# Performance work log

Measured on AMD Instinct MI355X. Metric: run time of the kernel, lower is better.

## Reference

```python
import jax, jax.numpy as jnp
import numpy as np

VL = 32

def setup_inputs() -> dict:
    key = jax.random.key(0)
    k1, k2, k3 = jax.random.split(key, 3)
    user = jax.random.normal(k1, (16384, 20, VL + 1), dtype=jnp.float32)
    ctx = jax.random.normal(k2, (16384, 10, VL + 1), dtype=jnp.float32)
    doc = jax.random.normal(k3, (16384, 30, VL + 1), dtype=jnp.float32)
    return {"user": user, "ctx": ctx, "doc": doc}

def reference(user, ctx, doc):
    # feats: [B, F, vl+1] where F = total field count across user/ctx/doc
    feats = jnp.concatenate([user, ctx, doc], axis=1)
    v = feats[..., :VL]          # [B, F, vl] latent factors
    linear = feats[..., -1]      # [B, F]   linear term (last column)
    # FM cross term: 0.5 * ((sum_f v)^2 - sum_f v^2), summed over latent dims
    sum_v = jnp.sum(v, axis=1)           # [B, vl]
    sum_v2 = jnp.sum(v * v, axis=1)      # [B, vl]
    cross = 0.5 * jnp.sum(sum_v * sum_v - sum_v2, axis=-1)  # [B]
    logits = cross + jnp.sum(linear, axis=1)                 # [B]
    return jax.nn.sigmoid(logits)
```

## Files before the change

### kernel.cpp

```cpp
#include <hip/hip_runtime.h>
#include <hip/hip_bf16.h>
#include <math.h>


#define NS 16384
#define PPB 4

__global__ __launch_bounds__(128) void fm_kernel(
    const float* __restrict__ user,
    const float* __restrict__ ctx,
    const float* __restrict__ doc,
    float* __restrict__ out) {
  __shared__ float smem[3960];

  const int tid = threadIdx.x;
  const int pair0 = blockIdx.x * PPB;

  float4* su = (float4*)smem;
  float4* sc = (float4*)(smem + 1320);
  float4* sd = (float4*)(smem + 1980);

  const bool pu = (256 + tid) < 330;
  const bool pc = (128 + tid) < 165;
  const bool pd = (384 + tid) < 495;

  float4 r0, r1, r2, r3, r4, r5, r6, r7, r8;

  auto LOAD = [&](int pair) {
    const float4* gu = (const float4*)(user + (size_t)(2 * pair) * 660);
    const float4* gc = (const float4*)(ctx  + (size_t)(2 * pair) * 330);
    const float4* gd = (const float4*)(doc  + (size_t)(2 * pair) * 990);
    r0 = gu[tid];
    r1 = gu[128 + tid];
    if (pu) r2 = gu[256 + tid];
    r3 = gc[tid];
    if (pc) r4 = gc[128 + tid];
    r5 = gd[tid];
    r6 = gd[128 + tid];
    r7 = gd[256 + tid];
    if (pd) r8 = gd[384 + tid];
  };
  auto STORE = [&]() {
    su[tid] = r0;
    su[128 + tid] = r1;
    if (pu) su[256 + tid] = r2;
    sc[tid] = r3;
    if (pc) sc[128 + tid] = r4;
    sd[tid] = r5;
    sd[128 + tid] = r6;
    sd[256 + tid] = r7;
    if (pd) sd[384 + tid] = r8;
  };

  LOAD(pair0);
  STORE();
  __syncthreads();

  const int w = tid >> 6;
  const int l = tid & 63;
  const int h = l >> 5;
  const int e = l & 31;

  const float* mu = smem + w * 660;
  const float* mc = smem + 1320 + w * 330;
  const float* md = smem + 1980 + w * 990;
  const float* p1 = (h ? md : mu) + e;
  const float* p2 = (h ? (md + 660) : mc) + e;

  for (int it = 0; it < PPB; ++it) {
    const bool more = (it + 1 < PPB);
    if (more) LOAD(pair0 + it + 1);

    float sv = 0.f, sv2 = 0.f;
#pragma unroll
    for (int f = 0; f < 20; ++f) {
      float x = p1[f * 33];
      sv += x; sv2 = fmaf(x, x, sv2);
    }
#pragma unroll
    for (int f = 0; f < 10; ++f) {
      float x = p2[f * 33];
      sv += x; sv2 = fmaf(x, x, sv2);
    }

    float lin = 0.f;
    if (h == 0) {
      if (e < 20)      lin = mu[e * 33 + 32];
      else if (e < 30) lin = mc[(e - 20) * 33 + 32];
    } else {
      if (e < 30) lin = md[e * 33 + 32];
    }

    float svT  = sv  + __shfl_xor(sv,  32, 64);
    float sv2T = sv2 + __shfl_xor(sv2, 32, 64);
    float linT = lin + __shfl_xor(lin, 32, 64);
    float part = fmaf(svT, svT, -sv2T);
#pragma unroll
    for (int m = 16; m > 0; m >>= 1) {
      part += __shfl_xor(part, m, 64);
      linT += __shfl_xor(linT, m, 64);
    }
    if (l == 0) {
      float logit = fmaf(0.5f, part, linT);
      out[2 * (pair0 + it) + w] = 1.f / (1.f + expf(-logit));
    }

    if (more) {
      __syncthreads();
      STORE();
      __syncthreads();
    }
  }
}

extern "C" void kernel_launch(void* const* d_in, const int* in_sizes, int n_in,
                              void* d_out, int out_size, void* d_ws, size_t ws_size,
                              hipStream_t stream) {
  const float* user = (const float*)d_in[0];
  const float* ctx  = (const float*)d_in[1];
  const float* doc  = (const float*)d_in[2];
  float* out = (float*)d_out;

  dim3 block(128);
  dim3 grid(NS / 2 / PPB);
  fm_kernel<<<grid, block, 0, stream>>>(user, ctx, doc, out);
}
```

Before: 144.9 us.

## Double-buffer LDS with direct global-to-LDS async loads and larger PPB

Replaces the register-staged global loads and LDS stores with global_load_lds builtins that write straight into a double-buffered shared-memory region. Each wave loads one half (user+ctx or doc) and the next pair is prefetched while the current one is computed, synchronised by vmcnt waits and raw barriers. Pairs per block go from 4 to 8, halving the grid. The goal is to remove the VGPR round trip and one barrier per iteration. The risks are the doubled LDS footprint, fewer blocks, and the ordering of the manual waitcnt.

```diff
diff --git a/kernel.cpp b/kernel.cpp
--- a/kernel.cpp
+++ b/kernel.cpp
@@ -1,75 +1,71 @@
 #include <hip/hip_runtime.h>
-#include <hip/hip_bf16.h>
 #include <math.h>
 
 
 #define NS 16384
-#define PPB 4
+#define PPB 8
+
+__device__ __forceinline__ void glds16(const void* g, void* l) {
+  __builtin_amdgcn_global_load_lds(
+      (const __attribute__((address_space(1))) void*)g,
+      (__attribute__((address_space(3))) void*)l,
+      16, 0, 0);
+}
 
 __global__ __launch_bounds__(128) void fm_kernel(
     const float* __restrict__ user,
     const float* __restrict__ ctx,
     const float* __restrict__ doc,
     float* __restrict__ out) {
-  __shared__ float smem[3960];
+  __shared__ float smem[2 * 3960];
 
-  const int tid = threadIdx.x;
+  const int tid  = threadIdx.x;
+  const int w    = tid >> 6;
+  const int lane = tid & 63;
   const int pair0 = blockIdx.x * PPB;
 
-  float4* su = (float4*)smem;
-  float4* sc = (float4*)(smem + 1320);
-  float4* sd = (float4*)(smem + 1980);
-
-  const bool pu = (256 + tid) < 330;
-  const bool pc = (128 + tid) < 165;
-  const bool pd = (384 + tid) < 495;
-
-  float4 r0, r1, r2, r3, r4, r5, r6, r7, r8;
-
-  auto LOAD = [&](int pair) {
-    const float4* gu = (const float4*)(user + (size_t)(2 * pair) * 660);
-    const float4* gc = (const float4*)(ctx  + (size_t)(2 * pair) * 330);
-    const float4* gd = (const float4*)(doc  + (size_t)(2 * pair) * 990);
-    r0 = gu[tid];
-    r1 = gu[128 + tid];
-    if (pu) r2 = gu[256 + tid];
-    r3 = gc[tid];
-    if (pc) r4 = gc[128 + tid];
-    r5 = gd[tid];
-    r6 = gd[128 + tid];
-    r7 = gd[256 + tid];
-    if (pd) r8 = gd[384 + tid];
-  };
-  auto STORE = [&]() {
-    su[tid] = r0;
-    su[128 + tid] = r1;
-    if (pu) su[256 + tid] = r2;
-    sc[tid] = r3;
-    if (pc) sc[128 + tid] = r4;
-    sd[tid] = r5;
-    sd[128 + tid] = r6;
-    sd[256 + tid] = r7;
-    if (pd) sd[384 + tid] = r8;
+  auto STAGE = [&](int cb, int pair) {
+    float* buf = smem + cb * 3960;
+    if (w == 0) {
+      const float4* gu = (const float4*)(user + (size_t)(2 * pair) * 660);
+      const float4* gc = (const float4*)(ctx  + (size_t)(2 * pair) * 330);
+#pragma unroll
+      for (int i = 0; i < 8; ++i) {
+        int k = i * 64 + lane;
+        const float4* src = (k < 330) ? (gu + k) : (gc + (k - 330));
+        if (k < 495) glds16(src, buf + i * 256);
+      }
+    } else {
+      const float4* gd = (const float4*)(doc + (size_t)(2 * pair) * 990);
+      float* dbase = buf + 1980;
+#pragma unroll
+      for (int i = 0; i < 8; ++i) {
+        int k = i * 64 + lane;
+        if (k < 495) glds16(gd + k, dbase + i * 256);
+      }
+    }
   };
 
-  LOAD(pair0);
-  STORE();
-  __syncthreads();
+  const int h = (lane >> 5);
+  const int e = lane & 31;
 
-  const int w = tid >> 6;
-  const int l = tid & 63;
-  const int h = l >> 5;
-  const int e = l & 31;
-
-  const float* mu = smem + w * 660;
-  const float* mc = smem + 1320 + w * 330;
-  const float* md = smem + 1980 + w * 990;
-  const float* p1 = (h ? md : mu) + e;
-  const float* p2 = (h ? (md + 660) : mc) + e;
+  STAGE(0, pair0);
 
   for (int it = 0; it < PPB; ++it) {
+    const int cur = it & 1;
     const bool more = (it + 1 < PPB);
-    if (more) LOAD(pair0 + it + 1);
+    if (more) STAGE(cur ^ 1, pair0 + it + 1);
+
+    if (more) asm volatile("s_waitcnt vmcnt(8)" ::: "memory");
+    else      asm volatile("s_waitcnt vmcnt(0)" ::: "memory");
+    __builtin_amdgcn_s_barrier();
+
+    const float* base = smem + cur * 3960;
+    const float* mu = base + w * 660;
+    const float* mc = base + 1320 + w * 330;
+    const float* md = base + 1980 + w * 990;
+    const float* p1 = (h ? md : mu) + e;
+    const float* p2 = (h ? (md + 660) : mc) + e;
 
     float sv = 0.f, sv2 = 0.f;
 #pragma unroll
@@ -100,16 +96,12 @@
       part += __shfl_xor(part, m, 64);
       linT += __shfl_xor(linT, m, 64);
     }
-    if (l == 0) {
+    if (lane == 0) {
       float logit = fmaf(0.5f, part, linT);
       out[2 * (pair0 + it) + w] = 1.f / (1.f + expf(-logit));
     }
 
-    if (more) {
-      __syncthreads();
-      STORE();
-      __syncthreads();
-    }
+    __builtin_amdgcn_s_barrier();
   }
 }
 
```

Measured after the change: 148.5 us. +2.5%, slower.
